# Performance work log

Hardware: AMD Instinct MI355X
Metric: run time of the kernel (lower is better)

Reference implementation:

```python
import jax, jax.numpy as jnp
import numpy as np

B, H0, W0, C = 16, 56, 56, 96
NH, WS, SS = 3, 7, 3
HID, NCL, TAU = 384, 128, 0.5
EPS = 1e-6

def layernorm(x, g, b):
    m = jnp.mean(x, -1, keepdims=True)
    v = jnp.mean((x - m) ** 2, -1, keepdims=True)
    return (x - m) * jax.lax.rsqrt(v + 1e-5) * g + b

def setup_inputs() -> dict:
    key = jax.random.key(0)
    ks = jax.random.split(key, 16)
    s = lambda d: 1.0 / np.sqrt(d)
    return {
        "x": jax.random.normal(ks[0], (B, H0 * W0, C), jnp.float32),
        "norm1_g": jnp.ones((C,)), "norm1_b": jnp.zeros((C,)),
        "qkv_w": jax.random.normal(ks[1], (3 * C, C)) * s(C),
        "qkv_b": jnp.zeros((3 * C,)),
        "proj_w": jax.random.normal(ks[2], (C, C)) * s(C),
        "proj_b": jnp.zeros((C,)),
        "norm2_g": jnp.ones((C,)), "norm2_b": jnp.zeros((C,)),
        "ffn_norm_g": jnp.ones((C,)), "ffn_norm_b": jnp.zeros((C,)),
        "pin_w": jax.random.normal(ks[3], (HID, C)) * s(C),
        "pin_b": jnp.zeros((HID,)),
        "tm_inc": jax.random.normal(ks[4], (NCL, 2 * HID)) * 0.5,
        "tm_out": jax.random.normal(ks[5], (NCL, C)) * s(NCL),
        "gate": jnp.float32(0.5),
        "H": H0, "W": W0,
    }

def window_attention(win, qkv_w, qkv_b, proj_w, proj_b):
    N, T, Cc = win.shape
    hd = Cc // NH
    qkv = win @ qkv_w.T + qkv_b                      # [N, T, 3C]
    qkv = qkv.reshape(N, T, 3, NH, hd).transpose(2, 0, 3, 1, 4)
    q, k, v = qkv[0], qkv[1], qkv[2]                 # [N, nh, T, hd]
    attn = jax.nn.softmax(jnp.einsum('nhqd,nhkd->nhqk', q, k) * (hd ** -0.5), axis=-1)
    out = jnp.einsum('nhqk,nhkd->nhqd', attn, v).transpose(0, 2, 1, 3).reshape(N, T, Cc)
    return out @ proj_w.T + proj_b

def tm_ffn(x, ffn_norm_g, ffn_norm_b, pin_w, pin_b, tm_inc, tm_out, gate):
    # x: [B, T, C]
    Bb, T, Cc = x.shape
    y = jax.nn.sigmoid(layernorm(x, ffn_norm_g, ffn_norm_b) @ pin_w.T + pin_b)  # [B,T,HID]
    flat = y.reshape(Bb * T, HID)
    lits = jnp.clip(jnp.concatenate([flat, 1.0 - flat], axis=-1), EPS, 1.0)     # [N, 2*HID]
    m = jax.nn.sigmoid(tm_inc)
    hard = (m > TAU).astype(m.dtype)
    m_ste = m + jax.lax.stop_gradient(hard - m)      # binary via STE
    # binary mask -> conjunction prod_k l_k^{m_jk} = exp(log(l) @ m^T)
    clauses = jnp.exp(jnp.log(lits) @ m_ste.T)       # [N, NCL]
    logits = (clauses @ tm_out).reshape(Bb, T, Cc)
    g = jax.nn.sigmoid(gate)
    return g * logits + (1.0 - g) * jax.nn.sigmoid(logits)

def reference(x, norm1_g, norm1_b, qkv_w, qkv_b, proj_w, proj_b,
              norm2_g, norm2_b, ffn_norm_g, ffn_norm_b,
              pin_w, pin_b, tm_inc, tm_out, gate, H, W):
    Bb, L, Cc = x.shape
    shortcut = x
    y = layernorm(x, norm1_g, norm1_b).reshape(Bb, H, W, Cc)
    pad_h = (WS - H % WS) % WS
    pad_w = (WS - W % WS) % WS
    if pad_h or pad_w:
        y = jnp.pad(y, ((0, 0), (0, pad_h), (0, pad_w), (0, 0)))
    Hp, Wp = y.shape[1], y.shape[2]
    if SS > 0:
        y = jnp.roll(y, shift=(-SS, -SS), axis=(1, 2))
    # window partition
    y = y.reshape(Bb, Hp // WS, WS, Wp // WS, WS, Cc).transpose(0, 1, 3, 2, 4, 5)
    win = y.reshape(-1, WS * WS, Cc)
    a = window_attention(win, qkv_w, qkv_b, proj_w, proj_b)
    a = a.reshape(Bb, Hp // WS, Wp // WS, WS, WS, Cc)
    if SS > 0:
        a = jnp.roll(a, shift=(SS, SS), axis=(3, 4))
    # window reverse
    a = a.transpose(0, 1, 3, 2, 4, 5).reshape(Bb, Hp, Wp, Cc)
    if pad_h or pad_w:
        a = a[:, :H, :W, :]
    a = a.reshape(Bb, H * W, Cc)
    x1 = shortcut + a
    x2 = x1 + tm_ffn(layernorm(x1, norm2_g, norm2_b),
                     ffn_norm_g, ffn_norm_b, pin_w, pin_b, tm_inc, tm_out, gate)
    return x2
```

## Files before the change

### kernel.cpp

```cpp
#include <hip/hip_runtime.h>

#define NB 16
#define NHH 56
#define NWW 56
#define NC 96
#define NL (NHH*NWW)
#define NTOK (NB*NL)
#define WSZ 7
#define NT 49
#define SSH 3
#define NWIN 1024
#define HDIM 32
#define HID_ 384
#define NCL_ 128
#define NLIT 768
#define EPS_ 1e-6f
#define LOG_EPS -13.815510558f

typedef unsigned short u16;
typedef unsigned int   u32;
typedef __attribute__((ext_vector_type(8))) short short8;
typedef __attribute__((ext_vector_type(4))) float f32x4;

__device__ __forceinline__ float us2f(u16 u) {
  union { u32 u; float f; } x; x.u = ((u32)u) << 16; return x.f;
}
__device__ __forceinline__ u16 f2us(float f) {
  union { float f; u32 u; } x; x.f = f;
  u32 lsb = (x.u >> 16) & 1u;
  return (u16)((x.u + 0x7fffu + lsb) >> 16);
}
__device__ __forceinline__ float sigmoidf_(float x) { return 1.f / (1.f + __expf(-x)); }

__global__ __launch_bounds__(256) void k0_prep(const float* __restrict__ tm_inc,
                                               const float* __restrict__ pin_w,
                                               const float* __restrict__ tm_out,
                                               const float* __restrict__ qkv_w,
                                               const float* __restrict__ proj_w,
                                               u16* __restrict__ maskb,
                                               u16* __restrict__ pinwb,
                                               u16* __restrict__ tmoT,
                                               u16* __restrict__ qkvwb,
                                               u16* __restrict__ projwb) {
  int idx = blockIdx.x * 256 + threadIdx.x;
  if (idx < NCL_ * NLIT)
    maskb[idx] = (tm_inc[idx] > 0.f) ? (u16)0x3F80 : (u16)0;
  if (idx < HID_ * NC)
    pinwb[idx] = f2us(pin_w[idx]);
  if (idx < NC * NCL_) {
    int c = idx / NCL_, k = idx - c * NCL_;
    tmoT[idx] = f2us(tm_out[(size_t)k * NC + c]);
  }
  if (idx < 3 * NC * NC)
    qkvwb[idx] = f2us(qkv_w[idx]);
  if (idx < NC * NC)
    projwb[idx] = f2us(proj_w[idx]);
}

__global__ __launch_bounds__(256) void k2_attn(const float* __restrict__ x,
                                               const float* __restrict__ n1g,
                                               const float* __restrict__ n1b,
                                               const u16* __restrict__ qkvwb,
                                               const float* __restrict__ qkv_b,
                                               const u16* __restrict__ projwb,
                                               const float* __restrict__ proj_b,
                                               float* __restrict__ x1) {
  __shared__ __align__(16) u16 syb[64 * 104];
  __shared__ __align__(16) u16 sk [64 * 104];
  __shared__ __align__(16) u16 svT[96 * 72];
  __shared__ __align__(16) u16 sp [4 * 16 * 72];
  const int tid  = threadIdx.x;
  const int wave = tid >> 6;
  const int lane = tid & 63;
  const int l16  = lane & 15;
  const int quad = lane >> 4;
  const int win  = blockIdx.x;
  const int t0   = wave * 16;
  const int bb = win >> 6, wl = win & 63;
  const int hbase = (wl >> 3) * WSZ, wbase = (wl & 7) * WSZ;

  {
    const int t = tid >> 2, s = tid & 3;
    if (t < NT) {
      int hp = hbase + t / WSZ, wp = wbase + t % WSZ;
      int h = hp + SSH; if (h >= NHH) h -= NHH;
      int w = wp + SSH; if (w >= NWW) w -= NWW;
      const float* xp = x + ((size_t)bb * NL + (size_t)h * NWW + w) * NC;
      float4 v[6];
      float sum = 0.f;
      #pragma unroll
      for (int k = 0; k < 6; ++k) {
        v[k] = *reinterpret_cast<const float4*>(xp + s * 4 + k * 16);
        sum += v[k].x + v[k].y + v[k].z + v[k].w;
      }
      sum += __shfl_xor(sum, 1); sum += __shfl_xor(sum, 2);
      float mean = sum * (1.f / 96.f);
      float ssq = 0.f;
      #pragma unroll
      for (int k = 0; k < 6; ++k) {
        float d0 = v[k].x - mean, d1 = v[k].y - mean;
        float d2 = v[k].z - mean, d3 = v[k].w - mean;
        ssq += d0 * d0 + d1 * d1 + d2 * d2 + d3 * d3;
      }
      ssq += __shfl_xor(ssq, 1); ssq += __shfl_xor(ssq, 2);
      float rstd = rsqrtf(ssq * (1.f / 96.f) + 1e-5f);
      #pragma unroll
      for (int k = 0; k < 6; ++k) {
        int c = s * 4 + k * 16;
        const float4 g4 = *reinterpret_cast<const float4*>(n1g + c);
        const float4 b4 = *reinterpret_cast<const float4*>(n1b + c);
        syb[t * 104 + c + 0] = f2us((v[k].x - mean) * rstd * g4.x + b4.x);
        syb[t * 104 + c + 1] = f2us((v[k].y - mean) * rstd * g4.y + b4.y);
        syb[t * 104 + c + 2] = f2us((v[k].z - mean) * rstd * g4.z + b4.z);
        syb[t * 104 + c + 3] = f2us((v[k].w - mean) * rstd * g4.w + b4.w);
      }
    } else {
      #pragma unroll
      for (int k = 0; k < 6; ++k) {
        int c = s * 4 + k * 16;
        syb[t * 104 + c + 0] = 0; syb[t * 104 + c + 1] = 0;
        syb[t * 104 + c + 2] = 0; syb[t * 104 + c + 3] = 0;
      }
    }
  }

  {
    short8 afr[3];
    #pragma unroll
    for (int ks = 0; ks < 3; ++ks)
      afr[ks] = *reinterpret_cast<const short8*>(&syb[(t0 + l16) * 104 + quad * 8 + ks * 32]);
    short8 rb[4][3];
    #pragma unroll
    for (int p = 0; p < 4; ++p)
      #pragma unroll
      for (int ks = 0; ks < 3; ++ks)
        rb[p][ks] = *reinterpret_cast<const short8*>(
            qkvwb + (size_t)(p * 16 + l16) * NC + quad * 8 + ks * 32);
    #pragma unroll
    for (int nt = 0; nt < 18; ++nt) {
      const int n0 = nt * 16;
      const float bias = qkv_b[n0 + l16];
      short8 b0 = rb[nt & 3][0], b1 = rb[nt & 3][1], b2 = rb[nt & 3][2];
      if (nt + 4 < 18) {
        #pragma unroll
        for (int ks = 0; ks < 3; ++ks)
          rb[nt & 3][ks] = *reinterpret_cast<const short8*>(
              qkvwb + (size_t)((nt + 4) * 16 + l16) * NC + quad * 8 + ks * 32);
      }
      f32x4 acc = {0.f, 0.f, 0.f, 0.f};
      acc = __builtin_amdgcn_mfma_f32_16x16x32_bf16(afr[0], b0, acc, 0, 0, 0);
      acc = __builtin_amdgcn_mfma_f32_16x16x32_bf16(afr[1], b1, acc, 0, 0, 0);
      acc = __builtin_amdgcn_mfma_f32_16x16x32_bf16(afr[2], b2, acc, 0, 0, 0);
      const int part = nt / 6;
      const int oc = n0 - part * 96 + l16;
      if (part < 2) {
        u16* dst = (part == 0) ? syb : sk;
        #pragma unroll
        for (int r = 0; r < 4; ++r)
          dst[(t0 + quad * 4 + r) * 104 + oc] = f2us(acc[r] + bias);
      } else {
        #pragma unroll
        for (int r = 0; r < 4; ++r)
          svT[oc * 72 + (t0 + quad * 4 + r)] = f2us(acc[r] + bias);
      }
    }
  }
  __syncthreads();

  u16* spw = sp + wave * 16 * 72;
  const float sscale = 0.17677669529663687f;
  short8 qf[3];
  f32x4 s[3][4];
  #pragma unroll
  for (int h = 0; h < 3; ++h)
    qf[h] = *reinterpret_cast<const short8*>(&syb[(t0 + l16) * 104 + h * HDIM + quad * 8]);
  #pragma unroll
  for (int h = 0; h < 3; ++h) {
    const int d0 = h * HDIM;
    #pragma unroll
    for (int nt = 0; nt < 4; ++nt) {
      short8 kf = *reinterpret_cast<const short8*>(&sk[(nt * 16 + l16) * 104 + d0 + quad * 8]);
      f32x4 a = {0.f, 0.f, 0.f, 0.f};
      s[h][nt] = __builtin_amdgcn_mfma_f32_16x16x32_bf16(qf[h], kf, a, 0, 0, 0);
    }
  }
  #pragma unroll
  for (int h = 0; h < 3; ++h) {
    const int d0 = h * HDIM;
    #pragma unroll
    for (int nt = 0; nt < 4; ++nt)
      #pragma unroll
      for (int r = 0; r < 4; ++r) s[h][nt][r] *= sscale;
    if (l16 >= 1) {
      #pragma unroll
      for (int r = 0; r < 4; ++r) s[h][3][r] = -1e30f;
    }
    #pragma unroll
    for (int r = 0; r < 4; ++r) {
      float m = fmaxf(fmaxf(s[h][0][r], s[h][1][r]), fmaxf(s[h][2][r], s[h][3][r]));
      #pragma unroll
      for (int off = 8; off > 0; off >>= 1) m = fmaxf(m, __shfl_xor(m, off, 16));
      float e0 = __expf(s[h][0][r] - m), e1 = __expf(s[h][1][r] - m);
      float e2 = __expf(s[h][2][r] - m), e3 = __expf(s[h][3][r] - m);
      float sum = e0 + e1 + e2 + e3;
      #pragma unroll
      for (int off = 8; off > 0; off >>= 1) sum += __shfl_xor(sum, off, 16);
      float inv = 1.f / sum;
      const int row = quad * 4 + r;
      spw[row * 72 +      l16] = f2us(e0 * inv);
      spw[row * 72 + 16 + l16] = f2us(e1 * inv);
      spw[row * 72 + 32 + l16] = f2us(e2 * inv);
      spw[row * 72 + 48 + l16] = f2us(e3 * inv);
    }
    short8 pa[2];
    pa[0] = *reinterpret_cast<const short8*>(&spw[l16 * 72 + quad * 8]);
    pa[1] = *reinterpret_cast<const short8*>(&spw[l16 * 72 + 32 + quad * 8]);
    #pragma unroll
    for (int nt = 0; nt < 2; ++nt) {
      const int c0 = d0 + nt * 16;
      f32x4 acc = {0.f, 0.f, 0.f, 0.f};
      #pragma unroll
      for (int ks = 0; ks < 2; ++ks) {
        short8 vb = *reinterpret_cast<const short8*>(&svT[(c0 + l16) * 72 + ks * 32 + quad * 8]);
        acc = __builtin_amdgcn_mfma_f32_16x16x32_bf16(pa[ks], vb, acc, 0, 0, 0);
      }
      #pragma unroll
      for (int r = 0; r < 4; ++r)
        syb[(t0 + quad * 4 + r) * 104 + c0 + l16] = f2us(acc[r]);
    }
  }

  {
    short8 aa[3];
    #pragma unroll
    for (int ks = 0; ks < 3; ++ks)
      aa[ks] = *reinterpret_cast<const short8*>(&syb[(t0 + l16) * 104 + quad * 8 + ks * 32]);

    size_t tokr[4]; bool tval[4];
    #pragma unroll
    for (int r = 0; r < 4; ++r) {
      const int t = t0 + quad * 4 + r;
      tval[r] = (t < NT);
      int rr = t / WSZ + SSH; if (rr >= WSZ) rr -= WSZ;
      int qq = t % WSZ + SSH; if (qq >= WSZ) qq -= WSZ;
      tokr[r] = (size_t)bb * NL + (size_t)(hbase + rr) * NWW + (wbase + qq);
    }
    float xv[6][4];
    #pragma unroll
    for (int nt = 0; nt < 6; ++nt)
      #pragma unroll
      for (int r = 0; r < 4; ++r)
        xv[nt][r] = tval[r] ? x[tokr[r] * NC + nt * 16 + l16] : 0.f;

    short8 pbr[2][3];
    #pragma unroll
    for (int ks = 0; ks < 3; ++ks)
      pbr[0][ks] = *reinterpret_cast<const short8*>(
          projwb + (size_t)l16 * NC + quad * 8 + ks * 32);
    #pragma unroll
    for (int nt = 0; nt < 6; ++nt) {
      const int n0 = nt * 16;
      const float pb = proj_b[n0 + l16];
      short8 b0 = pbr[nt & 1][0], b1 = pbr[nt & 1][1], b2 = pbr[nt & 1][2];
      if (nt + 1 < 6) {
        #pragma unroll
        for (int ks = 0; ks < 3; ++ks)
          pbr[(nt + 1) & 1][ks] = *reinterpret_cast<const short8*>(
              projwb + (size_t)((nt + 1) * 16 + l16) * NC + quad * 8 + ks * 32);
      }
      f32x4 acc = {0.f, 0.f, 0.f, 0.f};
      acc = __builtin_amdgcn_mfma_f32_16x16x32_bf16(aa[0], b0, acc, 0, 0, 0);
      acc = __builtin_amdgcn_mfma_f32_16x16x32_bf16(aa[1], b1, acc, 0, 0, 0);
      acc = __builtin_amdgcn_mfma_f32_16x16x32_bf16(aa[2], b2, acc, 0, 0, 0);
      #pragma unroll
      for (int r = 0; r < 4; ++r) {
        if (tval[r])
          x1[tokr[r] * NC + n0 + l16] = xv[nt][r] + acc[r] + pb;
      }
    }
  }
}

__global__ __launch_bounds__(512) void k4_ffn(const float* __restrict__ x1,
                                              const float* __restrict__ g2,
                                              const float* __restrict__ b2,
                                              const float* __restrict__ gf,
                                              const float* __restrict__ bf,
                                              const u16* __restrict__ pinwb,
                                              const float* __restrict__ pin_b,
                                              const u16* __restrict__ maskb,
                                              const u16* __restrict__ tmoT,
                                              const float* __restrict__ gate,
                                              float* __restrict__ out) {
  __shared__ __align__(16) u16 lit[32 * 776];
  __shared__ __align__(16) u16 su[32 * 136];
  u16* szb  = su;
  u16* claT = su;
  const int tid  = threadIdx.x;
  const int wave = tid >> 6;
  const int lane = tid & 63;
  const int l16  = lane & 15;
  const int quad = lane >> 4;
  const size_t tok0 = (size_t)blockIdx.x * 32;

  {
    const int t = tid >> 4, s = tid & 15;
    const float* xp = x1 + (tok0 + t) * NC;
    float2 v[3];
    float sum = 0.f;
    #pragma unroll
    for (int k = 0; k < 3; ++k) {
      const int c = s * 2 + k * 32;
      v[k] = *reinterpret_cast<const float2*>(xp + c);
      sum += v[k].x + v[k].y;
    }
    #pragma unroll
    for (int off = 8; off > 0; off >>= 1) sum += __shfl_xor(sum, off, 16);
    const float mean = sum * (1.f / 96.f);
    float ssq = 0.f;
    #pragma unroll
    for (int k = 0; k < 3; ++k) {
      float d0 = v[k].x - mean, d1 = v[k].y - mean;
      ssq += d0 * d0 + d1 * d1;
    }
    #pragma unroll
    for (int off = 8; off > 0; off >>= 1) ssq += __shfl_xor(ssq, off, 16);
    const float rstd = rsqrtf(ssq * (1.f / 96.f) + 1e-5f);
    float tv[6];
    float sum2 = 0.f;
    #pragma unroll
    for (int k = 0; k < 3; ++k) {
      const int c = s * 2 + k * 32;
      const float2 gg = *reinterpret_cast<const float2*>(g2 + c);
      const float2 bb = *reinterpret_cast<const float2*>(b2 + c);
      tv[2 * k]     = (v[k].x - mean) * rstd * gg.x + bb.x;
      tv[2 * k + 1] = (v[k].y - mean) * rstd * gg.y + bb.y;
      sum2 += tv[2 * k] + tv[2 * k + 1];
    }
    #pragma unroll
    for (int off = 8; off > 0; off >>= 1) sum2 += __shfl_xor(sum2, off, 16);
    const float mean2 = sum2 * (1.f / 96.f);
    float ssq2 = 0.f;
    #pragma unroll
    for (int k = 0; k < 3; ++k) {
      float d0 = tv[2 * k] - mean2, d1 = tv[2 * k + 1] - mean2;
      ssq2 += d0 * d0 + d1 * d1;
    }
    #pragma unroll
    for (int off = 8; off > 0; off >>= 1) ssq2 += __shfl_xor(ssq2, off, 16);
    const float rstd2 = rsqrtf(ssq2 * (1.f / 96.f) + 1e-5f);
    #pragma unroll
    for (int k = 0; k < 3; ++k) {
      const int c = s * 2 + k * 32;
      const float2 gg = *reinterpret_cast<const float2*>(gf + c);
      const float2 bb = *reinterpret_cast<const float2*>(bf + c);
      u16 lo = f2us((tv[2 * k]     - mean2) * rstd2 * gg.x + bb.x);
      u16 hi = f2us((tv[2 * k + 1] - mean2) * rstd2 * gg.y + bb.y);
      *reinterpret_cast<u32*>(&szb[t * 104 + c]) = (u32)lo | ((u32)hi << 16);
    }
  }
  __syncthreads();

  const float gv = sigmoidf_(gate[0]);

  short8 a_pin[2][3];
  #pragma unroll
  for (int mt = 0; mt < 2; ++mt)
    #pragma unroll
    for (int ks = 0; ks < 3; ++ks)
      a_pin[mt][ks] = *reinterpret_cast<const short8*>(
          &szb[(mt * 16 + l16) * 104 + quad * 8 + ks * 32]);

  {
    float pbias[3];
    #pragma unroll
    for (int i = 0; i < 3; ++i) pbias[i] = pin_b[(wave * 3 + i) * 16 + l16];
    short8 pb[3][3];
    #pragma unroll
    for (int i = 0; i < 3; ++i)
      #pragma unroll
      for (int ks = 0; ks < 3; ++ks)
        pb[i][ks] = *reinterpret_cast<const short8*>(
            pinwb + (size_t)((wave * 3 + i) * 16 + l16) * NC + quad * 8 + ks * 32);
    #pragma unroll
    for (int i = 0; i < 3; ++i) {
      f32x4 acc0 = {0.f, 0.f, 0.f, 0.f}, acc1 = {0.f, 0.f, 0.f, 0.f};
      acc0 = __builtin_amdgcn_mfma_f32_16x16x32_bf16(a_pin[0][0], pb[i][0], acc0, 0, 0, 0);
      acc1 = __builtin_amdgcn_mfma_f32_16x16x32_bf16(a_pin[1][0], pb[i][0], acc1, 0, 0, 0);
      acc0 = __builtin_amdgcn_mfma_f32_16x16x32_bf16(a_pin[0][1], pb[i][1], acc0, 0, 0, 0);
      acc1 = __builtin_amdgcn_mfma_f32_16x16x32_bf16(a_pin[1][1], pb[i][1], acc1, 0, 0, 0);
      acc0 = __builtin_amdgcn_mfma_f32_16x16x32_bf16(a_pin[0][2], pb[i][2], acc0, 0, 0, 0);
      acc1 = __builtin_amdgcn_mfma_f32_16x16x32_bf16(a_pin[1][2], pb[i][2], acc1, 0, 0, 0);
      const int o = (wave * 3 + i) * 16 + l16;
      const float pbv = pbias[i];
      #pragma unroll
      for (int r = 0; r < 4; ++r) {
        const float a0 = acc0[r] + pbv;
        const float sp0 = fmaxf(a0, 0.f) + __logf(1.f + __expf(-fabsf(a0)));
        const float a1 = acc1[r] + pbv;
        const float sp1 = fmaxf(a1, 0.f) + __logf(1.f + __expf(-fabsf(a1)));
        const int ta = quad * 4 + r, tb = 16 + quad * 4 + r;
        lit[ta * 776 + o]       = f2us(fmaxf(a0 - sp0, LOG_EPS));
        lit[ta * 776 + 384 + o] = f2us(fmaxf(-sp0, LOG_EPS));
        lit[tb * 776 + o]       = f2us(fmaxf(a1 - sp1, LOG_EPS));
        lit[tb * 776 + 384 + o] = f2us(fmaxf(-sp1, LOG_EPS));
      }
    }
  }
  __syncthreads();

  float xr[2][4];
  if (wave < 6) {
    const int c = wave * 16 + l16;
    #pragma unroll
    for (int r = 0; r < 4; ++r) {
      xr[0][r] = x1[(tok0 + quad * 4 + r) * NC + c];
      xr[1][r] = x1[(tok0 + 16 + quad * 4 + r) * NC + c];
    }
  }

  {
    const int ct = wave;
    const u16* bp0 = maskb + (size_t)(ct * 16 + l16) * NLIT + quad * 8;
    short8 rb0[8];
    #pragma unroll
    for (int p = 0; p < 8; ++p)
      rb0[p] = *reinterpret_cast<const short8*>(bp0 + p * 32);
    f32x4 c00 = {0.f, 0.f, 0.f, 0.f}, c10 = {0.f, 0.f, 0.f, 0.f};
    #pragma unroll
    for (int ks = 0; ks < 24; ++ks) {
      const int k0 = ks * 32 + quad * 8;
      short8 a0 = *reinterpret_cast<const short8*>(&lit[l16 * 776 + k0]);
      short8 a1 = *reinterpret_cast<const short8*>(&lit[(16 + l16) * 776 + k0]);
      short8 b0 = rb0[ks & 7];
      if (ks + 8 < 24)
        rb0[ks & 7] = *reinterpret_cast<const short8*>(bp0 + (ks + 8) * 32);
      c00 = __builtin_amdgcn_mfma_f32_16x16x32_bf16(a0, b0, c00, 0, 0, 0);
      c10 = __builtin_amdgcn_mfma_f32_16x16x32_bf16(a1, b0, c10, 0, 0, 0);
    }
    #pragma unroll
    for (int r = 0; r < 4; ++r) {
      const int ta = quad * 4 + r, tb = 16 + quad * 4 + r;
      claT[ta * 136 + ct * 16 + l16] = f2us(__expf(c00[r]));
      claT[tb * 136 + ct * 16 + l16] = f2us(__expf(c10[r]));
    }
  }
  __syncthreads();

  if (wave < 6) {
    const int nt = wave;
    short8 btm[4];
    #pragma unroll
    for (int ks = 0; ks < 4; ++ks)
      btm[ks] = *reinterpret_cast<const short8*>(
          tmoT + (size_t)(nt * 16 + l16) * NCL_ + ks * 32 + quad * 8);
    f32x4 acc0 = {0.f, 0.f, 0.f, 0.f}, acc1 = {0.f, 0.f, 0.f, 0.f};
    #pragma unroll
    for (int ks = 0; ks < 4; ++ks) {
      const int k0 = ks * 32 + quad * 8;
      short8 a0 = *reinterpret_cast<const short8*>(&claT[l16 * 136 + k0]);
      short8 a1 = *reinterpret_cast<const short8*>(&claT[(16 + l16) * 136 + k0]);
      acc0 = __builtin_amdgcn_mfma_f32_16x16x32_bf16(a0, btm[ks], acc0, 0, 0, 0);
      acc1 = __builtin_amdgcn_mfma_f32_16x16x32_bf16(a1, btm[ks], acc1, 0, 0, 0);
    }
    const int c = nt * 16 + l16;
    #pragma unroll
    for (int r = 0; r < 4; ++r) {
      const int ta = quad * 4 + r, tb = 16 + quad * 4 + r;
      float lg0 = acc0[r], lg1 = acc1[r];
      out[(tok0 + ta) * NC + c] = xr[0][r] + gv * lg0 + (1.f - gv) * sigmoidf_(lg0);
      out[(tok0 + tb) * NC + c] = xr[1][r] + gv * lg1 + (1.f - gv) * sigmoidf_(lg1);
    }
  }
}

extern "C" void kernel_launch(void* const* d_in, const int* in_sizes, int n_in,
                              void* d_out, int out_size, void* d_ws, size_t ws_size,
                              hipStream_t stream) {
  (void)in_sizes; (void)n_in; (void)out_size; (void)ws_size;
  const float* x      = (const float*)d_in[0];
  const float* n1g    = (const float*)d_in[1];
  const float* n1b    = (const float*)d_in[2];
  const float* qkv_w  = (const float*)d_in[3];
  const float* qkv_b  = (const float*)d_in[4];
  const float* proj_w = (const float*)d_in[5];
  const float* proj_b = (const float*)d_in[6];
  const float* n2g    = (const float*)d_in[7];
  const float* n2b    = (const float*)d_in[8];
  const float* fng    = (const float*)d_in[9];
  const float* fnb    = (const float*)d_in[10];
  const float* pin_w  = (const float*)d_in[11];
  const float* pin_b  = (const float*)d_in[12];
  const float* tm_inc = (const float*)d_in[13];
  const float* tm_out = (const float*)d_in[14];
  const float* gate   = (const float*)d_in[15];

  float* x1 = (float*)d_ws;
  u16* maskb = (u16*)(x1 + (size_t)NTOK * NC);
  u16* pinwb = maskb + NCL_ * NLIT;
  u16* tmoT  = pinwb + HID_ * NC;
  u16* qkvwb = tmoT + NC * NCL_;
  u16* projwb= qkvwb + 3 * NC * NC;

  hipLaunchKernelGGL(k0_prep, dim3(384), dim3(256), 0, stream,
                     tm_inc, pin_w, tm_out, qkv_w, proj_w, maskb, pinwb, tmoT, qkvwb, projwb);
  hipLaunchKernelGGL(k2_attn, dim3(NWIN), dim3(256), 0, stream,
                     x, n1g, n1b, qkvwb, qkv_b, projwb, proj_b, x1);
  hipLaunchKernelGGL(k4_ffn, dim3(NTOK / 32), dim3(512), 0, stream,
                     x1, n2g, n2b, fng, fnb, pinwb, pin_b, maskb, tmoT, gate, (float*)d_out);
}
```

Measured before the change: 196.2 us.

## Alias shared buffers and interleave literal layout to raise occupancy

Removes the separate softmax-probability buffer in the attention kernel by reusing the K buffer, and removes the su buffer in the FFN kernel by aliasing it onto the literal buffer. Extra barriers are added so the reused memory is only overwritten after it has been read. Literals are now stored interleaved (x, 1-x) and packed into 32-bit LDS stores, and the mask columns are permuted in the prep kernel to match. Launch bounds now request higher occupancy, which could force register spills in exchange for fewer LDS-limited blocks per CU.

```diff
diff --git a/kernel.cpp b/kernel.cpp
--- a/kernel.cpp
+++ b/kernel.cpp
@@ -43,8 +43,11 @@
                                                u16* __restrict__ qkvwb,
                                                u16* __restrict__ projwb) {
   int idx = blockIdx.x * 256 + threadIdx.x;
-  if (idx < NCL_ * NLIT)
-    maskb[idx] = (tm_inc[idx] > 0.f) ? (u16)0x3F80 : (u16)0;
+  if (idx < NCL_ * NLIT) {
+    int c = idx / NLIT, q = idx - c * NLIT;
+    int j = (q & 1) ? (q >> 1) + HID_ : (q >> 1);
+    maskb[idx] = (tm_inc[(size_t)c * NLIT + j] > 0.f) ? (u16)0x3F80 : (u16)0;
+  }
   if (idx < HID_ * NC)
     pinwb[idx] = f2us(pin_w[idx]);
   if (idx < NC * NCL_) {
@@ -57,7 +60,7 @@
     projwb[idx] = f2us(proj_w[idx]);
 }
 
-__global__ __launch_bounds__(256) void k2_attn(const float* __restrict__ x,
+__global__ __launch_bounds__(256, 4) void k2_attn(const float* __restrict__ x,
                                                const float* __restrict__ n1g,
                                                const float* __restrict__ n1b,
                                                const u16* __restrict__ qkvwb,
@@ -68,7 +71,6 @@
   __shared__ __align__(16) u16 syb[64 * 104];
   __shared__ __align__(16) u16 sk [64 * 104];
   __shared__ __align__(16) u16 svT[96 * 72];
-  __shared__ __align__(16) u16 sp [4 * 16 * 72];
   const int tid  = threadIdx.x;
   const int wave = tid >> 6;
   const int lane = tid & 63;
@@ -167,7 +169,7 @@
   }
   __syncthreads();
 
-  u16* spw = sp + wave * 16 * 72;
+  u16* spw = sk + wave * 16 * 72;
   const float sscale = 0.17677669529663687f;
   short8 qf[3];
   f32x4 s[3][4];
@@ -184,6 +186,7 @@
       s[h][nt] = __builtin_amdgcn_mfma_f32_16x16x32_bf16(qf[h], kf, a, 0, 0, 0);
     }
   }
+  __syncthreads();
   #pragma unroll
   for (int h = 0; h < 3; ++h) {
     const int d0 = h * HDIM;
@@ -281,7 +284,7 @@
   }
 }
 
-__global__ __launch_bounds__(512) void k4_ffn(const float* __restrict__ x1,
+__global__ __launch_bounds__(512, 6) void k4_ffn(const float* __restrict__ x1,
                                               const float* __restrict__ g2,
                                               const float* __restrict__ b2,
                                               const float* __restrict__ gf,
@@ -293,9 +296,8 @@
                                               const float* __restrict__ gate,
                                               float* __restrict__ out) {
   __shared__ __align__(16) u16 lit[32 * 776];
-  __shared__ __align__(16) u16 su[32 * 136];
-  u16* szb  = su;
-  u16* claT = su;
+  u16* szb  = lit;
+  u16* claT = lit;
   const int tid  = threadIdx.x;
   const int wave = tid >> 6;
   const int lane = tid & 63;
@@ -370,6 +372,7 @@
     for (int ks = 0; ks < 3; ++ks)
       a_pin[mt][ks] = *reinterpret_cast<const short8*>(
           &szb[(mt * 16 + l16) * 104 + quad * 8 + ks * 32]);
+  __syncthreads();
 
   {
     float pbias[3];
@@ -400,10 +403,12 @@
         const float a1 = acc1[r] + pbv;
         const float sp1 = fmaxf(a1, 0.f) + __logf(1.f + __expf(-fabsf(a1)));
         const int ta = quad * 4 + r, tb = 16 + quad * 4 + r;
-        lit[ta * 776 + o]       = f2us(fmaxf(a0 - sp0, LOG_EPS));
-        lit[ta * 776 + 384 + o] = f2us(fmaxf(-sp0, LOG_EPS));
-        lit[tb * 776 + o]       = f2us(fmaxf(a1 - sp1, LOG_EPS));
-        lit[tb * 776 + 384 + o] = f2us(fmaxf(-sp1, LOG_EPS));
+        const u16 lo0 = f2us(fmaxf(a0 - sp0, LOG_EPS));
+        const u16 hi0 = f2us(fmaxf(-sp0, LOG_EPS));
+        const u16 lo1 = f2us(fmaxf(a1 - sp1, LOG_EPS));
+        const u16 hi1 = f2us(fmaxf(-sp1, LOG_EPS));
+        *reinterpret_cast<u32*>(&lit[ta * 776 + 2 * o]) = (u32)lo0 | ((u32)hi0 << 16);
+        *reinterpret_cast<u32*>(&lit[tb * 776 + 2 * o]) = (u32)lo1 | ((u32)hi1 << 16);
       }
     }
   }
@@ -438,11 +443,15 @@
       c00 = __builtin_amdgcn_mfma_f32_16x16x32_bf16(a0, b0, c00, 0, 0, 0);
       c10 = __builtin_amdgcn_mfma_f32_16x16x32_bf16(a1, b0, c10, 0, 0, 0);
     }
+    float e0[4], e1[4];
+    #pragma unroll
+    for (int r = 0; r < 4; ++r) { e0[r] = __expf(c00[r]); e1[r] = __expf(c10[r]); }
+    __syncthreads();
     #pragma unroll
     for (int r = 0; r < 4; ++r) {
       const int ta = quad * 4 + r, tb = 16 + quad * 4 + r;
-      claT[ta * 136 + ct * 16 + l16] = f2us(__expf(c00[r]));
-      claT[tb * 136 + ct * 16 + l16] = f2us(__expf(c10[r]));
+      claT[ta * 136 + ct * 16 + l16] = f2us(e0[r]);
+      claT[tb * 136 + ct * 16 + l16] = f2us(e1[r]);
     }
   }
   __syncthreads();
```

After: 188.1 us (median of 2 runs). -4.1%, faster.
